# Kernel optimization log

Hardware: AMD Instinct MI355X
Metric: run time of the kernel (lower is better)

## Reference

```python
import jax, jax.numpy as jnp
import numpy as np
import math

NUM_BUCKETS = 32
MAX_DISTANCE = 128
N_HEADS = 16
HEAD_DIM = 64


def _relative_position_bucket(relative_position, num_buckets=NUM_BUCKETS, max_distance=MAX_DISTANCE):
    # bidirectional (encoder): half the buckets for positive positions
    nb = num_buckets // 2
    rel_buckets = (relative_position > 0).astype(jnp.int32) * nb
    rp = jnp.abs(relative_position)
    max_exact = nb // 2
    is_small = rp < max_exact
    rp_large = max_exact + (
        jnp.log(jnp.maximum(rp, 1).astype(jnp.float32) / max_exact)
        / math.log(max_distance / max_exact)
        * (nb - max_exact)
    ).astype(jnp.int32)
    rp_large = jnp.minimum(rp_large, nb - 1)
    return rel_buckets + jnp.where(is_small, rp, rp_large)


def setup_inputs() -> dict:
    key = jax.random.key(0)
    ks = jax.random.split(key, 6)
    d_model = 1024
    B, S = 4, 2048
    scale = 1.0 / math.sqrt(d_model)
    return {
        "hidden_states": jax.random.normal(ks[0], (B, S, d_model), jnp.float32),
        "Wq": jax.random.normal(ks[1], (d_model, N_HEADS * HEAD_DIM), jnp.float32) * scale,
        "Wk": jax.random.normal(ks[2], (d_model, N_HEADS * HEAD_DIM), jnp.float32) * scale,
        "Wv": jax.random.normal(ks[3], (d_model, N_HEADS * HEAD_DIM), jnp.float32) * scale,
        "Wo": jax.random.normal(ks[4], (N_HEADS * HEAD_DIM, d_model), jnp.float32) * scale,
        "rel_bias_table": jax.random.normal(ks[5], (NUM_BUCKETS, N_HEADS), jnp.float32),
    }


def reference(hidden_states, Wq, Wk, Wv, Wo, rel_bias_table):
    B, S, _ = hidden_states.shape
    # projections -> [B, H, S, hd]
    def proj(W):
        return jnp.einsum('bsd,df->bsf', hidden_states, W).reshape(B, S, N_HEADS, HEAD_DIM).transpose(0, 2, 1, 3)
    q = proj(Wq)
    k = proj(Wk)
    v = proj(Wv)

    # relative position bias: [1, H, S, S]
    ctx = jnp.arange(S)[:, None]
    mem = jnp.arange(S)[None, :]
    buckets = _relative_position_bucket(mem - ctx)  # [S, S] int32
    position_bias = rel_bias_table[buckets].transpose(2, 0, 1)[None]  # [1, H, S, S]

    # scaling = 1.0 in MT5Attention (d_kv**-0.5 baked into init elsewhere)
    attn_weights = jnp.einsum('bhqd,bhkd->bhqk', q, k) + position_bias
    attn_weights = jax.nn.softmax(attn_weights, axis=-1)
    attn_output = jnp.einsum('bhqk,bhkd->bqhd', attn_weights, v).reshape(B, S, N_HEADS * HEAD_DIM)
    attn_output = jnp.einsum('bsf,fd->bsd', attn_output, Wo)
    return attn_output, position_bias, attn_weights
```

## Files before the change

### kernel.cpp

```cpp
#include <hip/hip_runtime.h>
#include <cstdint>
#include <cmath>

#define NH 16
#define HD 64
#define SQ 2048
#define NB 4
#define DM 1024

typedef _Float16 half_t;
typedef _Float16 h8 __attribute__((ext_vector_type(8)));
typedef _Float16 h4 __attribute__((ext_vector_type(4)));
typedef float f4 __attribute__((ext_vector_type(4)));

__device__ __forceinline__ int rel_bucket(int delta) {
    int b = (delta > 0) ? 16 : 0;
    int a = (delta < 0) ? -delta : delta;
    if (a < 8) return b + a;
    int large = 8 + (int)(__logf((float)a * 0.125f) * 2.8853900817779268f);
    return b + (large < 15 ? large : 15);
}

__device__ __forceinline__ void gl_lds(const half_t* g, half_t* l) {
    __builtin_amdgcn_global_load_lds((const __attribute__((address_space(1))) unsigned int*)g,
                                     (__attribute__((address_space(3))) unsigned int*)l, 16, 0, 0);
}

__global__ __launch_bounds__(256) void prep(const float* __restrict__ X,
                                            const float* __restrict__ Wq,
                                            const float* __restrict__ Wk,
                                            const float* __restrict__ Wv,
                                            const float* __restrict__ Wo,
                                            half_t* __restrict__ Xh, half_t* __restrict__ Wqt,
                                            half_t* __restrict__ Wkt, half_t* __restrict__ Wvt,
                                            half_t* __restrict__ Wot) {
    const int id = blockIdx.x;
    if (id < 4096) {
        size_t i = ((size_t)id * 256 + threadIdx.x) * 8;
        float4 a = *(const float4*)&X[i];
        float4 b = *(const float4*)&X[i + 4];
        half_t t[8] = {(half_t)a.x, (half_t)a.y, (half_t)a.z, (half_t)a.w,
                       (half_t)b.x, (half_t)b.y, (half_t)b.z, (half_t)b.w};
        *(h8*)&Xh[i] = *(h8*)t;
        return;
    }
    __shared__ float T[64][65];
    const int t = id - 4096;
    const int which = t >> 8, tile = t & 255;
    const float* W = which == 0 ? Wq : which == 1 ? Wk : which == 2 ? Wv : Wo;
    half_t* Wt = which == 0 ? Wqt : which == 1 ? Wkt : which == 2 ? Wvt : Wot;
    const int k0 = (tile >> 4) * 64, n0 = (tile & 15) * 64;
    const int c = threadIdx.x & 63, rr = threadIdx.x >> 6;
    for (int r = rr; r < 64; r += 4) T[r][c] = W[(size_t)(k0 + r) * DM + n0 + c];
    __syncthreads();
    for (int r = rr; r < 64; r += 4) Wt[(size_t)(n0 + r) * DM + k0 + c] = (half_t)T[c][r];
}

__global__ __launch_bounds__(256) void transpose_v(const half_t* __restrict__ v,
                                                   half_t* __restrict__ vT) {
    __shared__ half_t T[64][72];
    const int bh = blockIdx.y, j0 = blockIdx.x * 64;
    const size_t base = (size_t)bh * (SQ * HD);
    const int t = threadIdx.x;
    for (int e = t; e < 512; e += 256) {
        int r = e >> 3, c = e & 7;
        *(h8*)&T[r][c * 8] = *(const h8*)&v[base + (size_t)(j0 + r) * HD + c * 8];
    }
    __syncthreads();
    const int d = t & 63, jc = t >> 6;
    half_t tmp[16];
#pragma unroll
    for (int jj = 0; jj < 16; ++jj) tmp[jj] = T[jc * 16 + jj][d];
    *(h8*)&vT[base + (size_t)d * SQ + j0 + jc * 16] = *(h8*)&tmp[0];
    *(h8*)&vT[base + (size_t)d * SQ + j0 + jc * 16 + 8] = *(h8*)&tmp[8];
}

__global__ __launch_bounds__(256) void mm_qkv(const half_t* __restrict__ A,
                                              const half_t* __restrict__ Wqt,
                                              const half_t* __restrict__ Wkt,
                                              const half_t* __restrict__ Wvt,
                                              half_t* __restrict__ qo, half_t* __restrict__ ko,
                                              half_t* __restrict__ vo) {
    const int z = blockIdx.z;
    const half_t* Bt = z == 0 ? Wqt : z == 1 ? Wkt : Wvt;
    half_t* outp = z == 0 ? qo : z == 1 ? ko : vo;
    __shared__ half_t Al[2][4096];
    __shared__ half_t Bl[2][4096];
    const int tid = threadIdx.x;
    const int lane = tid & 63, w = tid >> 6;
    const int wr = w >> 1, wc = w & 1;
    const int m0 = blockIdx.y * 128, n0 = blockIdx.x * 128;

    f4 acc[4][4];
#pragma unroll
    for (int i = 0; i < 4; ++i)
#pragma unroll
        for (int j = 0; j < 4; ++j) acc[i][j] = (f4){0.f, 0.f, 0.f, 0.f};

    const int kc = lane >> 4;
    const int srl = lane >> 2;
    const int sc = lane & 3;

    auto stage = [&](int buf, int k0) {
#pragma unroll
        for (int inst = 0; inst < 2; ++inst) {
            int r = w * 32 + inst * 16 + srl;
            int cg = sc ^ ((r >> 1) & 3);
            gl_lds(&A[(size_t)(m0 + r) * DM + k0 + cg * 8], &Al[buf][(w * 32 + inst * 16) * 32]);
            gl_lds(&Bt[(size_t)(n0 + r) * DM + k0 + cg * 8], &Bl[buf][(w * 32 + inst * 16) * 32]);
        }
    };

    stage(0, 0);
    __syncthreads();
    int cur = 0;
    for (int t = 0; t < 32; ++t) {
        if (t < 31) stage(cur ^ 1, (t + 1) * 32);
        h8 af[4], bf[4];
#pragma unroll
        for (int ms = 0; ms < 4; ++ms) {
            int r = wr * 64 + ms * 16 + (lane & 15);
            af[ms] = *(const h8*)&Al[cur][r * 32 + ((kc ^ ((r >> 1) & 3)) * 8)];
        }
#pragma unroll
        for (int ns = 0; ns < 4; ++ns) {
            int r = wc * 64 + ns * 16 + (lane & 15);
            bf[ns] = *(const h8*)&Bl[cur][r * 32 + ((kc ^ ((r >> 1) & 3)) * 8)];
        }
#pragma unroll
        for (int ms = 0; ms < 4; ++ms)
#pragma unroll
            for (int ns = 0; ns < 4; ++ns)
                acc[ms][ns] =
                    __builtin_amdgcn_mfma_f32_16x16x32_f16(af[ms], bf[ns], acc[ms][ns], 0, 0, 0);
        __syncthreads();
        cur ^= 1;
    }

#pragma unroll
    for (int ms = 0; ms < 4; ++ms)
#pragma unroll
        for (int ns = 0; ns < 4; ++ns)
#pragma unroll
            for (int reg = 0; reg < 4; ++reg) {
                int m = m0 + wr * 64 + ms * 16 + (lane >> 4) * 4 + reg;
                int n = n0 + wc * 64 + ns * 16 + (lane & 15);
                int b = m >> 11, s = m & 2047, h = n >> 6, d = n & 63;
                outp[((size_t)(b * NH + h) * SQ + s) * HD + d] = (half_t)acc[ms][ns][reg];
            }
}

__global__ __launch_bounds__(256) void mm_wo(const half_t* __restrict__ A,
                                             const half_t* __restrict__ Bt,
                                             float* __restrict__ outp) {
    __shared__ half_t Al[2][4096];
    __shared__ half_t Bl[2][4096];
    const int tid = threadIdx.x;
    const int lane = tid & 63, w = tid >> 6;
    const int wr = w >> 1, wc = w & 1;
    const int m0 = blockIdx.y * 128, n0 = blockIdx.x * 128;

    f4 acc[4][4];
#pragma unroll
    for (int i = 0; i < 4; ++i)
#pragma unroll
        for (int j = 0; j < 4; ++j) acc[i][j] = (f4){0.f, 0.f, 0.f, 0.f};

    const int kc = lane >> 4;
    const int srl = lane >> 2;
    const int sc = lane & 3;

    auto stage = [&](int buf, int k0) {
#pragma unroll
        for (int inst = 0; inst < 2; ++inst) {
            int r = w * 32 + inst * 16 + srl;
            int cg = sc ^ ((r >> 1) & 3);
            gl_lds(&A[(size_t)(m0 + r) * DM + k0 + cg * 8], &Al[buf][(w * 32 + inst * 16) * 32]);
            gl_lds(&Bt[(size_t)(n0 + r) * DM + k0 + cg * 8], &Bl[buf][(w * 32 + inst * 16) * 32]);
        }
    };

    stage(0, 0);
    __syncthreads();
    int cur = 0;
    for (int t = 0; t < 32; ++t) {
        if (t < 31) stage(cur ^ 1, (t + 1) * 32);
        h8 af[4], bf[4];
#pragma unroll
        for (int ms = 0; ms < 4; ++ms) {
            int r = wr * 64 + ms * 16 + (lane & 15);
            af[ms] = *(const h8*)&Al[cur][r * 32 + ((kc ^ ((r >> 1) & 3)) * 8)];
        }
#pragma unroll
        for (int ns = 0; ns < 4; ++ns) {
            int r = wc * 64 + ns * 16 + (lane & 15);
            bf[ns] = *(const h8*)&Bl[cur][r * 32 + ((kc ^ ((r >> 1) & 3)) * 8)];
        }
#pragma unroll
        for (int ms = 0; ms < 4; ++ms)
#pragma unroll
            for (int ns = 0; ns < 4; ++ns)
                acc[ms][ns] =
                    __builtin_amdgcn_mfma_f32_16x16x32_f16(af[ms], bf[ns], acc[ms][ns], 0, 0, 0);
        __syncthreads();
        cur ^= 1;
    }

#pragma unroll
    for (int ms = 0; ms < 4; ++ms)
#pragma unroll
        for (int ns = 0; ns < 4; ++ns)
#pragma unroll
            for (int reg = 0; reg < 4; ++reg) {
                int m = m0 + wr * 64 + ms * 16 + (lane >> 4) * 4 + reg;
                int n = n0 + wc * 64 + ns * 16 + (lane & 15);
                __builtin_nontemporal_store(acc[ms][ns][reg], &outp[(size_t)m * DM + n]);
            }
}

__global__ __launch_bounds__(256) void fused_attn(const half_t* __restrict__ q,
                                                  const half_t* __restrict__ k,
                                                  const half_t* __restrict__ vT,
                                                  const float* __restrict__ table,
                                                  float* __restrict__ attw,
                                                  half_t* __restrict__ ctx) {
    __shared__ float biasE[2176];
    __shared__ char Psm[16384];
    __shared__ half_t Kl[2][4096];
    __shared__ half_t Vl[2][4096];
    const int tid = threadIdx.x, lane = tid & 63, w = tid >> 6;

    const int id = blockIdx.x;
    const int idx = (id & 7) * 128 + (id >> 3);
    const int bh = idx >> 4, i0 = (idx & 15) * 128;
    const int h = bh & 15, b = bh >> 4;
    const size_t qb = (size_t)bh * (SQ * HD);
    const half_t* kb = k + qb;
    const half_t* vb = vT + qb;

    for (int t = tid; t < 2176; t += 256)
        biasE[t] = __expf(table[rel_bucket(t - i0 - 127) * NH + h]);

    h8 qf[2][2];
#pragma unroll
    for (int isub = 0; isub < 2; ++isub) {
        const half_t* qp =
            &q[qb + (size_t)(i0 + w * 32 + isub * 16 + (lane & 15)) * HD + (lane >> 4) * 8];
        qf[isub][0] = *(const h8*)qp;
        qf[isub][1] = *(const h8*)(qp + 32);
    }

    const int sr = lane >> 3;
    const int sc = lane & 7;

    auto stageK = [&](int buf, int j0) {
#pragma unroll
        for (int inst = 0; inst < 2; ++inst) {
            int r = w * 16 + inst * 8 + sr;
            gl_lds(&kb[(size_t)(j0 + r) * HD + ((sc ^ (r & 7)) * 8)],
                   &Kl[buf][(w * 16 + inst * 8) * 64]);
        }
    };
    auto stageV = [&](int buf, int j0) {
#pragma unroll
        for (int inst = 0; inst < 2; ++inst) {
            int r = w * 16 + inst * 8 + sr;
            gl_lds(&vb[(size_t)r * SQ + j0 + ((sc ^ (r & 7)) * 8)],
                   &Vl[buf][(w * 16 + inst * 8) * 64]);
        }
    };

    stageK(0, 0);
    __syncthreads();
    float srow[2] = {0.f, 0.f};
    int cur = 0;
    for (int t = 0; t < 32; ++t) {
        const int j0 = t * 64;
        if (t < 31) stageK(cur ^ 1, j0 + 64);
#pragma unroll
        for (int ns = 0; ns < 4; ++ns) {
            const int rr = ns * 16 + (lane & 15);
            const int kc = lane >> 4;
            h8 kf0 = *(const h8*)&Kl[cur][rr * 64 + ((kc ^ (rr & 7)) * 8)];
            h8 kf1 = *(const h8*)&Kl[cur][rr * 64 + (((kc + 4) ^ (rr & 7)) * 8)];
#pragma unroll
            for (int isub = 0; isub < 2; ++isub) {
                f4 z = (f4){0.f, 0.f, 0.f, 0.f};
                z = __builtin_amdgcn_mfma_f32_16x16x32_f16(kf0, qf[isub][0], z, 0, 0, 0);
                z = __builtin_amdgcn_mfma_f32_16x16x32_f16(kf1, qf[isub][1], z, 0, 0, 0);
                int u0 =
                    j0 + ns * 16 + ((lane >> 4) << 2) - (w * 32 + isub * 16 + (lane & 15)) + 127;
#pragma unroll
                for (int reg = 0; reg < 4; ++reg)
                    srow[isub] = fmaf(__expf(z[reg]), biasE[u0 + reg], srow[isub]);
            }
        }
        __syncthreads();
        cur ^= 1;
    }
    float sinv[2];
#pragma unroll
    for (int isub = 0; isub < 2; ++isub) {
        float s = srow[isub];
        s += __shfl_xor(s, 16);
        s += __shfl_xor(s, 32);
        sinv[isub] = 1.0f / s;
    }

    f4 o[4][2];
#pragma unroll
    for (int ns = 0; ns < 4; ++ns)
#pragma unroll
        for (int isub = 0; isub < 2; ++isub) o[ns][isub] = (f4){0.f, 0.f, 0.f, 0.f};
    const size_t awb = (size_t)bh * ((size_t)SQ * SQ);
    char* Pw = Psm + w * 4096;

    stageK(0, 0);
    stageV(0, 0);
    __syncthreads();
    cur = 0;
    for (int t = 0; t < 32; ++t) {
        const int j0 = t * 64;
        if (t < 31) {
            stageK(cur ^ 1, j0 + 64);
            stageV(cur ^ 1, j0 + 64);
        }
        __builtin_amdgcn_sched_barrier(0);
        f4 a[4][2];
#pragma unroll
        for (int ns = 0; ns < 4; ++ns) {
            const int rr = ns * 16 + (lane & 15);
            const int kc = lane >> 4;
            h8 kf0 = *(const h8*)&Kl[cur][rr * 64 + ((kc ^ (rr & 7)) * 8)];
            h8 kf1 = *(const h8*)&Kl[cur][rr * 64 + (((kc + 4) ^ (rr & 7)) * 8)];
#pragma unroll
            for (int isub = 0; isub < 2; ++isub) {
                f4 z = (f4){0.f, 0.f, 0.f, 0.f};
                z = __builtin_amdgcn_mfma_f32_16x16x32_f16(kf0, qf[isub][0], z, 0, 0, 0);
                z = __builtin_amdgcn_mfma_f32_16x16x32_f16(kf1, qf[isub][1], z, 0, 0, 0);
                a[ns][isub] = z;
            }
        }
#pragma unroll
        for (int ns = 0; ns < 4; ++ns)
#pragma unroll
            for (int isub = 0; isub < 2; ++isub) {
                const int wloc = w * 32 + isub * 16 + (lane & 15);
                const int jbase = ns * 16 + ((lane >> 4) << 2);
                const int u0 = j0 + jbase - wloc + 127;
                f4 p;
#pragma unroll
                for (int reg = 0; reg < 4; ++reg)
                    p[reg] = __expf(a[ns][isub][reg]) * biasE[u0 + reg] * sinv[isub];
                __builtin_nontemporal_store(p,
                                            (f4*)&attw[awb + (size_t)(i0 + wloc) * SQ + j0 + jbase]);
                const int iloc = isub * 16 + (lane & 15);
                h4 ph = {(half_t)p[0], (half_t)p[1], (half_t)p[2], (half_t)p[3]};
                *(h4*)&Pw[iloc * 128 + (((jbase >> 3) ^ (iloc & 7)) << 4) + ((jbase & 4) << 1)] = ph;
            }
        h8 pf[2][2];
#pragma unroll
        for (int isub = 0; isub < 2; ++isub) {
            const int iloc = isub * 16 + (lane & 15);
            pf[isub][0] = *(const h8*)&Pw[iloc * 128 + (((lane >> 4) ^ (iloc & 7)) << 4)];
            pf[isub][1] = *(const h8*)&Pw[iloc * 128 + ((((lane >> 4) + 4) ^ (iloc & 7)) << 4)];
        }
#pragma unroll
        for (int ns = 0; ns < 4; ++ns) {
            const int rr = ns * 16 + (lane & 15);
            const int kc = lane >> 4;
            h8 vf0 = *(const h8*)&Vl[cur][rr * 64 + ((kc ^ (rr & 7)) * 8)];
            h8 vf1 = *(const h8*)&Vl[cur][rr * 64 + (((kc + 4) ^ (rr & 7)) * 8)];
#pragma unroll
            for (int isub = 0; isub < 2; ++isub) {
                o[ns][isub] =
                    __builtin_amdgcn_mfma_f32_16x16x32_f16(pf[isub][0], vf0, o[ns][isub], 0, 0, 0);
                o[ns][isub] =
                    __builtin_amdgcn_mfma_f32_16x16x32_f16(pf[isub][1], vf1, o[ns][isub], 0, 0, 0);
            }
        }
        asm volatile("s_waitcnt vmcnt(8)" ::: "memory");
        __builtin_amdgcn_s_barrier();
        __builtin_amdgcn_sched_barrier(0);
        cur ^= 1;
    }
#pragma unroll
    for (int ns = 0; ns < 4; ++ns)
#pragma unroll
        for (int isub = 0; isub < 2; ++isub)
#pragma unroll
            for (int reg = 0; reg < 4; ++reg) {
                int row = i0 + w * 32 + isub * 16 + (lane >> 4) * 4 + reg;
                int d = ns * 16 + (lane & 15);
                ctx[((size_t)(b * SQ + row)) * DM + h * HD + d] = (half_t)o[ns][isub][reg];
            }
}

__global__ __launch_bounds__(256) void bias_fill(const float* __restrict__ table,
                                                 float* __restrict__ pb) {
    __shared__ float t[512];
    const int tid = threadIdx.x;
    t[tid] = table[tid];
    t[tid + 256] = table[tid + 256];
    __syncthreads();
    const int i = blockIdx.x;
    const int h = blockIdx.y;
    const size_t base = ((size_t)h * SQ + i) * SQ;
#pragma unroll
    for (int half = 0; half < 2; ++half) {
        int j = half * 1024 + tid * 4;
        f4 o;
        o[0] = t[rel_bucket(j + 0 - i) * NH + h];
        o[1] = t[rel_bucket(j + 1 - i) * NH + h];
        o[2] = t[rel_bucket(j + 2 - i) * NH + h];
        o[3] = t[rel_bucket(j + 3 - i) * NH + h];
        __builtin_nontemporal_store(o, (f4*)&pb[base + j]);
    }
}

extern "C" void kernel_launch(void* const* d_in, const int* in_sizes, int n_in, void* d_out,
                              int out_size, void* d_ws, size_t ws_size, hipStream_t stream) {
    const float* X = (const float*)d_in[0];
    const float* Wq = (const float*)d_in[1];
    const float* Wk = (const float*)d_in[2];
    const float* Wv = (const float*)d_in[3];
    const float* Wo = (const float*)d_in[4];
    const float* tbl = (const float*)d_in[5];

    float* out = (float*)d_out;
    float* attn_out = out;
    float* pb = out + (size_t)NB * SQ * DM;
    float* attw = pb + (size_t)NH * SQ * SQ;

    const size_t need_bytes = 109051904;
    half_t* hb = (ws_size >= need_bytes) ? (half_t*)d_ws : (half_t*)pb;
    half_t* Xh = hb;
    half_t* qh = hb + 8388608;
    half_t* kh = hb + 16777216;
    half_t* vh = hb + 25165824;
    half_t* vTh = hb + 33554432;
    half_t* ctxh = hb + 41943040;
    half_t* Wqt = hb + 50331648;
    half_t* Wkt = hb + 51380224;
    half_t* Wvt = hb + 52428800;
    half_t* Wot = hb + 53477376;

    dim3 blk(256);
    prep<<<dim3(5120), blk, 0, stream>>>(X, Wq, Wk, Wv, Wo, Xh, Wqt, Wkt, Wvt, Wot);
    mm_qkv<<<dim3(8, 64, 3), blk, 0, stream>>>(Xh, Wqt, Wkt, Wvt, qh, kh, vh);
    transpose_v<<<dim3(32, 64), blk, 0, stream>>>(vh, vTh);
    fused_attn<<<dim3(1024), blk, 0, stream>>>(qh, kh, vTh, tbl, attw, ctxh);
    mm_wo<<<dim3(8, 64), blk, 0, stream>>>(ctxh, Wot, attn_out);
    bias_fill<<<dim3(SQ, NH), blk, 0, stream>>>(tbl, pb);
}
```

Baseline: 550.3 us.

## Precompute diagonal bias table, swizzle GEMM blocks, vectorize GEMM epilogue stores

The prep kernel now builds a per-head bias table indexed by relative distance (4095 entries). bias_fill copies a window of that table into LDS and reads it directly, so it no longer computes rel_bucket with a log for every element. Both projection GEMMs swap the MFMA operand order so each lane holds four consecutive columns, which allows 4-wide vector stores in the epilogue instead of scalar ones. The GEMM block index is also swizzled to improve L2 reuse. The cost is a small extra workspace and 16 more prep blocks.

```diff
diff --git a/kernel.cpp b/kernel.cpp
--- a/kernel.cpp
+++ b/kernel.cpp
@@ -31,9 +31,10 @@
                                             const float* __restrict__ Wk,
                                             const float* __restrict__ Wv,
                                             const float* __restrict__ Wo,
+                                            const float* __restrict__ table,
                                             half_t* __restrict__ Xh, half_t* __restrict__ Wqt,
                                             half_t* __restrict__ Wkt, half_t* __restrict__ Wvt,
-                                            half_t* __restrict__ Wot) {
+                                            half_t* __restrict__ Wot, float* __restrict__ dtab) {
     const int id = blockIdx.x;
     if (id < 4096) {
         size_t i = ((size_t)id * 256 + threadIdx.x) * 8;
@@ -42,6 +43,12 @@
         half_t t[8] = {(half_t)a.x, (half_t)a.y, (half_t)a.z, (half_t)a.w,
                        (half_t)b.x, (half_t)b.y, (half_t)b.z, (half_t)b.w};
         *(h8*)&Xh[i] = *(h8*)t;
+        return;
+    }
+    if (id >= 5120) {
+        const int h = id - 5120;
+        for (int d = threadIdx.x; d < 4095; d += 256)
+            dtab[h * 4096 + d] = table[rel_bucket(d - 2047) * NH + h];
         return;
     }
     __shared__ float T[64][65];
@@ -89,7 +96,9 @@
     const int tid = threadIdx.x;
     const int lane = tid & 63, w = tid >> 6;
     const int wr = w >> 1, wc = w & 1;
-    const int m0 = blockIdx.y * 128, n0 = blockIdx.x * 128;
+    const int id0 = blockIdx.y * 8 + blockIdx.x;
+    const int swz = (id0 & 7) * 64 + (id0 >> 3);
+    const int m0 = (swz >> 3) * 128, n0 = (swz & 7) * 128;
 
     f4 acc[4][4];
 #pragma unroll
@@ -132,7 +141,7 @@
 #pragma unroll
             for (int ns = 0; ns < 4; ++ns)
                 acc[ms][ns] =
-                    __builtin_amdgcn_mfma_f32_16x16x32_f16(af[ms], bf[ns], acc[ms][ns], 0, 0, 0);
+                    __builtin_amdgcn_mfma_f32_16x16x32_f16(bf[ns], af[ms], acc[ms][ns], 0, 0, 0);
         __syncthreads();
         cur ^= 1;
     }
@@ -140,14 +149,14 @@
 #pragma unroll
     for (int ms = 0; ms < 4; ++ms)
 #pragma unroll
-        for (int ns = 0; ns < 4; ++ns)
-#pragma unroll
-            for (int reg = 0; reg < 4; ++reg) {
-                int m = m0 + wr * 64 + ms * 16 + (lane >> 4) * 4 + reg;
-                int n = n0 + wc * 64 + ns * 16 + (lane & 15);
-                int b = m >> 11, s = m & 2047, h = n >> 6, d = n & 63;
-                outp[((size_t)(b * NH + h) * SQ + s) * HD + d] = (half_t)acc[ms][ns][reg];
-            }
+        for (int ns = 0; ns < 4; ++ns) {
+            int m = m0 + wr * 64 + ms * 16 + (lane & 15);
+            int nb = n0 + wc * 64 + ns * 16 + ((lane >> 4) << 2);
+            int b = m >> 11, s = m & 2047, h = nb >> 6, d = nb & 63;
+            h4 ph = {(half_t)acc[ms][ns][0], (half_t)acc[ms][ns][1], (half_t)acc[ms][ns][2],
+                     (half_t)acc[ms][ns][3]};
+            *(h4*)&outp[((size_t)(b * NH + h) * SQ + s) * HD + d] = ph;
+        }
 }
 
 __global__ __launch_bounds__(256) void mm_wo(const half_t* __restrict__ A,
@@ -158,7 +167,9 @@
     const int tid = threadIdx.x;
     const int lane = tid & 63, w = tid >> 6;
     const int wr = w >> 1, wc = w & 1;
-    const int m0 = blockIdx.y * 128, n0 = blockIdx.x * 128;
+    const int id0 = blockIdx.y * 8 + blockIdx.x;
+    const int swz = (id0 & 7) * 64 + (id0 >> 3);
+    const int m0 = (swz >> 3) * 128, n0 = (swz & 7) * 128;
 
     f4 acc[4][4];
 #pragma unroll
@@ -201,7 +212,7 @@
 #pragma unroll
             for (int ns = 0; ns < 4; ++ns)
                 acc[ms][ns] =
-                    __builtin_amdgcn_mfma_f32_16x16x32_f16(af[ms], bf[ns], acc[ms][ns], 0, 0, 0);
+                    __builtin_amdgcn_mfma_f32_16x16x32_f16(bf[ns], af[ms], acc[ms][ns], 0, 0, 0);
         __syncthreads();
         cur ^= 1;
     }
@@ -209,13 +220,11 @@
 #pragma unroll
     for (int ms = 0; ms < 4; ++ms)
 #pragma unroll
-        for (int ns = 0; ns < 4; ++ns)
-#pragma unroll
-            for (int reg = 0; reg < 4; ++reg) {
-                int m = m0 + wr * 64 + ms * 16 + (lane >> 4) * 4 + reg;
-                int n = n0 + wc * 64 + ns * 16 + (lane & 15);
-                __builtin_nontemporal_store(acc[ms][ns][reg], &outp[(size_t)m * DM + n]);
-            }
+        for (int ns = 0; ns < 4; ++ns) {
+            int m = m0 + wr * 64 + ms * 16 + (lane & 15);
+            int nb = n0 + wc * 64 + ns * 16 + ((lane >> 4) << 2);
+            __builtin_nontemporal_store(acc[ms][ns], (f4*)&outp[(size_t)m * DM + nb]);
+        }
 }
 
 __global__ __launch_bounds__(256) void fused_attn(const half_t* __restrict__ q,
@@ -396,24 +405,19 @@
             }
 }
 
-__global__ __launch_bounds__(256) void bias_fill(const float* __restrict__ table,
+__global__ __launch_bounds__(256) void bias_fill(const float* __restrict__ dtab,
                                                  float* __restrict__ pb) {
-    __shared__ float t[512];
-    const int tid = threadIdx.x;
-    t[tid] = table[tid];
-    t[tid + 256] = table[tid + 256];
-    __syncthreads();
-    const int i = blockIdx.x;
-    const int h = blockIdx.y;
+    __shared__ float L[2052];
+    const int i = blockIdx.x, h = blockIdx.y;
+    const int s0 = 2047 - i, a0 = s0 & ~3, sh = s0 - a0;
+    for (int t = threadIdx.x * 4; t < 2052; t += 1024)
+        *(f4*)&L[t] = *(const f4*)&dtab[h * 4096 + a0 + t];
+    __syncthreads();
     const size_t base = ((size_t)h * SQ + i) * SQ;
 #pragma unroll
     for (int half = 0; half < 2; ++half) {
-        int j = half * 1024 + tid * 4;
-        f4 o;
-        o[0] = t[rel_bucket(j + 0 - i) * NH + h];
-        o[1] = t[rel_bucket(j + 1 - i) * NH + h];
-        o[2] = t[rel_bucket(j + 2 - i) * NH + h];
-        o[3] = t[rel_bucket(j + 3 - i) * NH + h];
+        int j = half * 1024 + threadIdx.x * 4;
+        f4 o = {L[sh + j], L[sh + j + 1], L[sh + j + 2], L[sh + j + 3]};
         __builtin_nontemporal_store(o, (f4*)&pb[base + j]);
     }
 }
@@ -432,7 +436,7 @@
     float* pb = out + (size_t)NB * SQ * DM;
     float* attw = pb + (size_t)NH * SQ * SQ;
 
-    const size_t need_bytes = 109051904;
+    const size_t need_bytes = 109314048;
     half_t* hb = (ws_size >= need_bytes) ? (half_t*)d_ws : (half_t*)pb;
     half_t* Xh = hb;
     half_t* qh = hb + 8388608;
@@ -444,12 +448,13 @@
     half_t* Wkt = hb + 51380224;
     half_t* Wvt = hb + 52428800;
     half_t* Wot = hb + 53477376;
+    float* dtab = (float*)(hb + 54525952);
 
     dim3 blk(256);
-    prep<<<dim3(5120), blk, 0, stream>>>(X, Wq, Wk, Wv, Wo, Xh, Wqt, Wkt, Wvt, Wot);
+    prep<<<dim3(5136), blk, 0, stream>>>(X, Wq, Wk, Wv, Wo, tbl, Xh, Wqt, Wkt, Wvt, Wot, dtab);
     mm_qkv<<<dim3(8, 64, 3), blk, 0, stream>>>(Xh, Wqt, Wkt, Wvt, qh, kh, vh);
     transpose_v<<<dim3(32, 64), blk, 0, stream>>>(vh, vTh);
     fused_attn<<<dim3(1024), blk, 0, stream>>>(qh, kh, vTh, tbl, attw, ctxh);
     mm_wo<<<dim3(8, 64), blk, 0, stream>>>(ctxh, Wot, attn_out);
-    bias_fill<<<dim3(SQ, NH), blk, 0, stream>>>(tbl, pb);
-}
+    bias_fill<<<dim3(SQ, NH), blk, 0, stream>>>(dtab, pb);
+}
```

New measurement: 542.6 us. Within noise of the previous version (-1.4%).
